# Performance work log

Measured on AMD Instinct MI355X. Metric: run time of the kernel, lower is better.

Reference implementation:

```python
import jax, jax.numpy as jnp
import numpy as np

INV_SQRT2 = 0.7071067811865476  # Haar/db1 filter coefficient
LEVEL = 3


def _split(x, axis):
    """One Haar analysis step along `axis` (even length assumed)."""
    ax = axis % x.ndim
    sl0 = [slice(None)] * x.ndim; sl0[ax] = slice(0, None, 2)
    sl1 = [slice(None)] * x.ndim; sl1[ax] = slice(1, None, 2)
    x0, x1 = x[tuple(sl0)], x[tuple(sl1)]
    return (x0 + x1) * INV_SQRT2, (x0 - x1) * INV_SQRT2


def _merge(lo, hi, axis):
    """One Haar synthesis step along `axis` (interleave even/odd)."""
    ax = axis % lo.ndim
    e = (lo + hi) * INV_SQRT2
    o = (lo - hi) * INV_SQRT2
    s = jnp.stack([e, o], axis=ax + 1)
    shape = list(lo.shape)
    shape[ax] *= 2
    return s.reshape(shape)


def _dwt2(x):
    lo, hi = _split(x, -1)
    a, h = _split(lo, -2)
    v, d = _split(hi, -2)
    return a, h, v, d


def _idwt2(a, h, v, d):
    lo = _merge(a, h, -2)
    hi = _merge(v, d, -2)
    return _merge(lo, hi, -1)


def setup_inputs() -> dict:
    key = jax.random.key(0)
    ks = jax.random.split(key, 8)
    B, H, W = 16, 1024, 1024
    x = jax.random.normal(ks[0], (B, H, W, 1), dtype=jnp.float32)
    na = (H // 8) * (W // 8)   # approx size at level 3
    n2 = (H // 4) * (W // 4)
    n1 = (H // 2) * (W // 2)
    scale = 0.02
    Wa = jax.random.normal(ks[1], (na, 1), dtype=jnp.float32) * scale
    ba = jnp.zeros((1,), jnp.float32)
    Wd1 = jax.random.normal(ks[2], (3 * na, 3), dtype=jnp.float32) * scale  # coarsest details
    bd1 = jnp.zeros((3,), jnp.float32)
    Wd2 = jax.random.normal(ks[3], (3 * n2, 3), dtype=jnp.float32) * scale
    bd2 = jnp.zeros((3,), jnp.float32)
    Wd3 = jax.random.normal(ks[4], (3 * n1, 3), dtype=jnp.float32) * scale  # finest details
    bd3 = jnp.zeros((3,), jnp.float32)
    return {"x": x, "Wa": Wa, "ba": ba, "Wd1": Wd1, "bd1": bd1,
            "Wd2": Wd2, "bd2": bd2, "Wd3": Wd3, "bd3": bd3}


def reference(x, Wa, ba, Wd1, bd1, Wd2, bd2, Wd3, bd3):
    img = x[..., 0]                      # [B, H, W]
    B = img.shape[0]
    details = []                         # finest -> coarsest
    cur = img
    for _ in range(LEVEL):
        cur, h, v, d = _dwt2(cur)
        details.append((h, v, d))
    # approximation attention: sigmoid(Dense(1)) scalar gate per sample
    aw = jax.nn.sigmoid(cur.reshape(B, -1) @ Wa + ba)   # [B, 1]
    rec = cur * aw[:, :, None]                           # [B, H/8, W/8]
    # detail attention per level (coarsest first, matching pywt coeff order)
    det_params = [(Wd1, bd1), (Wd2, bd2), (Wd3, bd3)]
    for (h, v, d), (Wd, bd) in zip(reversed(details), det_params):
        flat = jnp.stack([h, v, d], axis=1).reshape(B, -1)      # [B, 3*hl*wl]
        w = jax.nn.softmax(flat @ Wd + bd, axis=-1)             # [B, 3]
        rec = _idwt2(rec,
                     h * w[:, 0, None, None],
                     v * w[:, 1, None, None],
                     d * w[:, 2, None, None])
    return rec                                                   # [B, H, W]
```

## Files before the change

kernel.cpp:

```cpp
#include <hip/hip_runtime.h>
#include <math.h>

#define HH 1024
#define WW 1024
#define N1 262144
#define N2 65536
#define N3 16384
#define NCHUNK 4
#define ROWS_PER_IMG 512

#define C_INV_SQRT2 0.70710678118654752440f

static __device__ __forceinline__ void haar_fwd(float P, float Q, float R, float S,
                                                float& a, float& h, float& v, float& d) {
    const float C = C_INV_SQRT2;
    float lo0 = (P + Q) * C, lo1 = (R + S) * C;
    float hi0 = (P - Q) * C, hi1 = (R - S) * C;
    a = (lo0 + lo1) * C; h = (lo0 - lo1) * C;
    v = (hi0 + hi1) * C; d = (hi0 - hi1) * C;
}

static __device__ __forceinline__ void haar_inv(float a, float h, float v, float d,
                                                float& P, float& Q, float& R, float& S) {
    const float C = C_INV_SQRT2;
    float elo = (a + h) * C, olo = (a - h) * C;
    float ehi = (v + d) * C, ohi = (v - d) * C;
    P = (elo + ehi) * C; Q = (elo - ehi) * C;
    R = (olo + ohi) * C; S = (olo - ohi) * C;
}

__global__ __launch_bounds__(256) void wa_fwd_dots(
    const float* __restrict__ x,
    const float* __restrict__ Wa,
    const float* __restrict__ Wd1,
    const float* __restrict__ Wd2,
    const float* __restrict__ Wd3,
    float* __restrict__ partial,
    int ipc)
{
    const int strip = blockIdx.x;
    const int chunk = blockIdx.y;
    const int t = threadIdx.x;
    const int lane = t & 63, wave = t >> 6;

    float w1[3][4][6];
    #pragma unroll
    for (int qr = 0; qr < 4; ++qr) {
        const size_t jj = (size_t)(strip * 4 + qr) * 512 + 2 * t;
        #pragma unroll
        for (int s = 0; s < 3; ++s) {
            const float2* src = (const float2*)(Wd3 + (jj + (size_t)s * N1) * 3);
            float2 f0 = src[0], f1 = src[1], f2 = src[2];
            w1[s][qr][0] = f0.x; w1[s][qr][1] = f0.y; w1[s][qr][2] = f1.x;
            w1[s][qr][3] = f1.y; w1[s][qr][4] = f2.x; w1[s][qr][5] = f2.y;
        }
    }
    float w2[3][2][3];
    #pragma unroll
    for (int QR = 0; QR < 2; ++QR) {
        const size_t jj = (size_t)(strip * 2 + QR) * 256 + t;
        #pragma unroll
        for (int s = 0; s < 3; ++s) {
            const float* src = Wd2 + (jj + (size_t)s * N2) * 3;
            w2[s][QR][0] = src[0]; w2[s][QR][1] = src[1]; w2[s][QR][2] = src[2];
        }
    }
    float w3[3][3] = {};
    float wa = 0.f;
    if (!(t & 1)) {
        const size_t jj = (size_t)strip * 128 + (t >> 1);
        wa = Wa[jj];
        #pragma unroll
        for (int s = 0; s < 3; ++s) {
            const float* src = Wd1 + (jj + (size_t)s * N3) * 3;
            w3[s][0] = src[0]; w3[s][1] = src[1]; w3[s][2] = src[2];
        }
    }

    #pragma unroll 2
    for (int bi = 0; bi < ipc; ++bi) {
        const int b = chunk * ipc + bi;
        const float* xr = x + (size_t)b * HH * WW + (size_t)strip * 8 * WW + 4 * t;

        float acc[10];
        #pragma unroll
        for (int c = 0; c < 10; ++c) acc[c] = 0.f;

        float a1[4][2];
        #pragma unroll
        for (int qr = 0; qr < 4; ++qr) {
            float4 u0 = *(const float4*)(xr + (size_t)(2 * qr)     * WW);
            float4 u1 = *(const float4*)(xr + (size_t)(2 * qr + 1) * WW);
            float h_[2], v_[2], d_[2];
            haar_fwd(u0.x, u0.y, u1.x, u1.y, a1[qr][0], h_[0], v_[0], d_[0]);
            haar_fwd(u0.z, u0.w, u1.z, u1.w, a1[qr][1], h_[1], v_[1], d_[1]);
            #pragma unroll
            for (int qc = 0; qc < 2; ++qc)
                #pragma unroll
                for (int c = 0; c < 3; ++c)
                    acc[7 + c] += h_[qc] * w1[0][qr][qc * 3 + c]
                                + v_[qc] * w1[1][qr][qc * 3 + c]
                                + d_[qc] * w1[2][qr][qc * 3 + c];
        }

        float a2[2];
        #pragma unroll
        for (int QR = 0; QR < 2; ++QR) {
            float h2, v2, d2;
            haar_fwd(a1[2 * QR][0], a1[2 * QR][1], a1[2 * QR + 1][0], a1[2 * QR + 1][1],
                     a2[QR], h2, v2, d2);
            #pragma unroll
            for (int c = 0; c < 3; ++c)
                acc[4 + c] += h2 * w2[0][QR][c] + v2 * w2[1][QR][c] + d2 * w2[2][QR][c];
        }

        {
            float oa0 = __shfl_xor(a2[0], 1);
            float oa1 = __shfl_xor(a2[1], 1);
            if (!(t & 1)) {
                float a3, h3, v3, d3;
                haar_fwd(a2[0], oa0, a2[1], oa1, a3, h3, v3, d3);
                acc[0] += a3 * wa;
                #pragma unroll
                for (int c = 0; c < 3; ++c)
                    acc[1 + c] += h3 * w3[0][c] + v3 * w3[1][c] + d3 * w3[2][c];
            }
        }

        #pragma unroll
        for (int c = 0; c < 10; ++c) {
            float s = acc[c];
            #pragma unroll
            for (int off = 1; off < 64; off <<= 1) s += __shfl_xor(s, off);
            acc[c] = s;
        }
        if (lane == 0) {
            float* row = partial + ((size_t)b * ROWS_PER_IMG + (size_t)strip * 4 + wave) * 10;
            #pragma unroll
            for (int c = 0; c < 10; ++c) row[c] = acc[c];
        }
    }
}

__global__ __launch_bounds__(64) void wa_gates(
    const float* __restrict__ partial,
    const float* __restrict__ ba,
    const float* __restrict__ bd1,
    const float* __restrict__ bd2,
    const float* __restrict__ bd3,
    float* __restrict__ gates)
{
    const int b = blockIdx.x;
    const int l = threadIdx.x;
    float v[10];
    #pragma unroll
    for (int c = 0; c < 10; ++c) v[c] = 0.f;
    for (int r = l; r < ROWS_PER_IMG; r += 64) {
        const float* row = partial + ((size_t)b * ROWS_PER_IMG + r) * 10;
        #pragma unroll
        for (int c = 0; c < 10; ++c) v[c] += row[c];
    }
    #pragma unroll
    for (int c = 0; c < 10; ++c) {
        #pragma unroll
        for (int off = 1; off < 64; off <<= 1) v[c] += __shfl_xor(v[c], off);
    }
    if (l == 0) {
        float* G = gates + b * 10;
        G[0] = 1.f / (1.f + expf(-(v[0] + ba[0])));
        const float* bds[3] = { bd1, bd2, bd3 };
        #pragma unroll
        for (int lv = 0; lv < 3; ++lv) {
            float l0 = v[1 + 3 * lv + 0] + bds[lv][0];
            float l1 = v[1 + 3 * lv + 1] + bds[lv][1];
            float l2 = v[1 + 3 * lv + 2] + bds[lv][2];
            float m = fmaxf(l0, fmaxf(l1, l2));
            float e0 = expf(l0 - m), e1 = expf(l1 - m), e2 = expf(l2 - m);
            float inv = 1.f / (e0 + e1 + e2);
            G[1 + 3 * lv + 0] = e0 * inv;
            G[1 + 3 * lv + 1] = e1 * inv;
            G[1 + 3 * lv + 2] = e2 * inv;
        }
    }
}

__global__ __launch_bounds__(256) void wa_recon(
    const float* __restrict__ x,
    const float* __restrict__ gates,
    float* __restrict__ out)
{
    const int strip = blockIdx.x;
    const int b = blockIdx.y;
    const int t = threadIdx.x;

    __shared__ float g[10];
    if (t < 10) g[t] = gates[b * 10 + t];
    __syncthreads();

    const float* xr = x + (size_t)b * HH * WW + (size_t)strip * 8 * WW + 4 * t;

    float a1[4][2], h1[4][2], v1[4][2], d1[4][2];
    #pragma unroll
    for (int qr = 0; qr < 4; ++qr) {
        float4 u0 = *(const float4*)(xr + (size_t)(2 * qr)     * WW);
        float4 u1 = *(const float4*)(xr + (size_t)(2 * qr + 1) * WW);
        haar_fwd(u0.x, u0.y, u1.x, u1.y, a1[qr][0], h1[qr][0], v1[qr][0], d1[qr][0]);
        haar_fwd(u0.z, u0.w, u1.z, u1.w, a1[qr][1], h1[qr][1], v1[qr][1], d1[qr][1]);
    }
    float a2[2], h2[2], v2[2], d2[2];
    #pragma unroll
    for (int QR = 0; QR < 2; ++QR)
        haar_fwd(a1[2 * QR][0], a1[2 * QR][1], a1[2 * QR + 1][0], a1[2 * QR + 1][1],
                 a2[QR], h2[QR], v2[QR], d2[QR]);

    float oa0 = __shfl_xor(a2[0], 1);
    float oa1 = __shfl_xor(a2[1], 1);
    const bool rightside = t & 1;
    float a3, h3, v3, d3;
    if (!rightside) haar_fwd(a2[0], oa0, a2[1], oa1, a3, h3, v3, d3);
    else            haar_fwd(oa0, a2[0], oa1, a2[1], a3, h3, v3, d3);

    a3 *= g[0];
    float P, Q, R, S;
    haar_inv(a3, h3 * g[1], v3 * g[2], d3 * g[3], P, Q, R, S);
    float r2[2];
    r2[0] = rightside ? Q : P;
    r2[1] = rightside ? S : R;

    float ra1[4][2];
    #pragma unroll
    for (int QR = 0; QR < 2; ++QR) {
        haar_inv(r2[QR], h2[QR] * g[4], v2[QR] * g[5], d2[QR] * g[6], P, Q, R, S);
        ra1[2 * QR][0] = P; ra1[2 * QR][1] = Q;
        ra1[2 * QR + 1][0] = R; ra1[2 * QR + 1][1] = S;
    }

    float* orow = out + (size_t)b * HH * WW + (size_t)strip * 8 * WW + 4 * t;
    #pragma unroll
    for (int qr = 0; qr < 4; ++qr) {
        float4 o0, o1;
        haar_inv(ra1[qr][0], h1[qr][0] * g[7], v1[qr][0] * g[8], d1[qr][0] * g[9],
                 o0.x, o0.y, o1.x, o1.y);
        haar_inv(ra1[qr][1], h1[qr][1] * g[7], v1[qr][1] * g[8], d1[qr][1] * g[9],
                 o0.z, o0.w, o1.z, o1.w);
        *(float4*)(orow + (size_t)(2 * qr)     * WW) = o0;
        *(float4*)(orow + (size_t)(2 * qr + 1) * WW) = o1;
    }
}

extern "C" void kernel_launch(void* const* d_in, const int* in_sizes, int n_in,
                              void* d_out, int out_size, void* d_ws, size_t ws_size,
                              hipStream_t stream) {
    const float* x   = (const float*)d_in[0];
    const float* Wa  = (const float*)d_in[1];
    const float* ba  = (const float*)d_in[2];
    const float* Wd1 = (const float*)d_in[3];
    const float* bd1 = (const float*)d_in[4];
    const float* Wd2 = (const float*)d_in[5];
    const float* bd2 = (const float*)d_in[6];
    const float* Wd3 = (const float*)d_in[7];
    const float* bd3 = (const float*)d_in[8];
    float* out = (float*)d_out;

    const int B = in_sizes[0] / (HH * WW);

    float* partial = (float*)d_ws;
    float* gates   = partial + (size_t)B * ROWS_PER_IMG * 10;

    int nchunk = NCHUNK, ipc = B / NCHUNK;
    if (B % NCHUNK) { nchunk = B; ipc = 1; }

    dim3 fgrid(128, nchunk);
    wa_fwd_dots<<<fgrid, 256, 0, stream>>>(x, Wa, Wd1, Wd2, Wd3, partial, ipc);
    wa_gates<<<B, 64, 0, stream>>>(partial, ba, bd1, bd2, bd3, gates);
    dim3 rgrid(128, B);
    wa_recon<<<rgrid, 256, 0, stream>>>(x, gates, out);
}
```

Before: 155.7 us.

## Fuse forward dots, gates and reconstruction into one cooperative kernel

```diff
diff --git a/kernel.cpp b/kernel.cpp
--- a/kernel.cpp
+++ b/kernel.cpp
@@ -1,5 +1,8 @@
 #include <hip/hip_runtime.h>
+#include <hip/hip_cooperative_groups.h>
 #include <math.h>
+
+namespace cg = cooperative_groups;
 
 #define HH 1024
 #define WW 1024
@@ -7,7 +10,7 @@
 #define N2 65536
 #define N3 16384
 #define NCHUNK 4
-#define ROWS_PER_IMG 512
+#define ROWS_PER_IMG 128
 
 #define C_INV_SQRT2 0.70710678118654752440f
 
@@ -27,6 +30,227 @@
     float ehi = (v + d) * C, ohi = (v - d) * C;
     P = (elo + ehi) * C; Q = (elo - ehi) * C;
     R = (olo + ohi) * C; S = (olo - ohi) * C;
+}
+
+static __device__ __forceinline__ void gates_from_partials(
+    const float* __restrict__ partial, int b, int lane,
+    const float* __restrict__ ba, const float* __restrict__ bd1,
+    const float* __restrict__ bd2, const float* __restrict__ bd3,
+    float* gdst)
+{
+    const float* base = partial + (size_t)b * ROWS_PER_IMG * 10 + lane * 20;
+    float v[10];
+    #pragma unroll
+    for (int c = 0; c < 10; ++c) v[c] = base[c] + base[10 + c];
+    #pragma unroll
+    for (int c = 0; c < 10; ++c) {
+        #pragma unroll
+        for (int off = 1; off < 64; off <<= 1) v[c] += __shfl_xor(v[c], off);
+    }
+    if (lane == 0) {
+        gdst[0] = 1.f / (1.f + expf(-(v[0] + ba[0])));
+        const float* bds[3] = { bd1, bd2, bd3 };
+        #pragma unroll
+        for (int lv = 0; lv < 3; ++lv) {
+            float l0 = v[1 + 3 * lv + 0] + bds[lv][0];
+            float l1 = v[1 + 3 * lv + 1] + bds[lv][1];
+            float l2 = v[1 + 3 * lv + 2] + bds[lv][2];
+            float m = fmaxf(l0, fmaxf(l1, l2));
+            float e0 = expf(l0 - m), e1 = expf(l1 - m), e2 = expf(l2 - m);
+            float inv = 1.f / (e0 + e1 + e2);
+            gdst[1 + 3 * lv + 0] = e0 * inv;
+            gdst[1 + 3 * lv + 1] = e1 * inv;
+            gdst[1 + 3 * lv + 2] = e2 * inv;
+        }
+    }
+}
+
+__global__ __launch_bounds__(256) void wa_fused(
+    const float* __restrict__ x,
+    const float* __restrict__ Wa,
+    const float* __restrict__ ba,
+    const float* __restrict__ bd1,
+    const float* __restrict__ bd2,
+    const float* __restrict__ bd3,
+    const float* __restrict__ Wd1,
+    const float* __restrict__ Wd2,
+    const float* __restrict__ Wd3,
+    float* __restrict__ out,
+    float* __restrict__ partial,
+    int ipc)
+{
+    const int strip = blockIdx.x;
+    const int chunk = blockIdx.y;
+    const int t = threadIdx.x;
+    const int lane = t & 63, wave = t >> 6;
+
+    __shared__ float red[4][10];
+    __shared__ float g_lds[16][10];
+
+    float w1[3][4][6];
+    #pragma unroll
+    for (int qr = 0; qr < 4; ++qr) {
+        const size_t jj = (size_t)(strip * 4 + qr) * 512 + 2 * t;
+        #pragma unroll
+        for (int s = 0; s < 3; ++s) {
+            const float2* src = (const float2*)(Wd3 + (jj + (size_t)s * N1) * 3);
+            float2 f0 = src[0], f1 = src[1], f2 = src[2];
+            w1[s][qr][0] = f0.x; w1[s][qr][1] = f0.y; w1[s][qr][2] = f1.x;
+            w1[s][qr][3] = f1.y; w1[s][qr][4] = f2.x; w1[s][qr][5] = f2.y;
+        }
+    }
+    float w2[3][2][3];
+    #pragma unroll
+    for (int QR = 0; QR < 2; ++QR) {
+        const size_t jj = (size_t)(strip * 2 + QR) * 256 + t;
+        #pragma unroll
+        for (int s = 0; s < 3; ++s) {
+            const float* src = Wd2 + (jj + (size_t)s * N2) * 3;
+            w2[s][QR][0] = src[0]; w2[s][QR][1] = src[1]; w2[s][QR][2] = src[2];
+        }
+    }
+    float w3[3][3] = {};
+    float wa = 0.f;
+    if (!(t & 1)) {
+        const size_t jj = (size_t)strip * 128 + (t >> 1);
+        wa = Wa[jj];
+        #pragma unroll
+        for (int s = 0; s < 3; ++s) {
+            const float* src = Wd1 + (jj + (size_t)s * N3) * 3;
+            w3[s][0] = src[0]; w3[s][1] = src[1]; w3[s][2] = src[2];
+        }
+    }
+
+    for (int bi = 0; bi < ipc; ++bi) {
+        const int b = chunk * ipc + bi;
+        const float* xr = x + (size_t)b * HH * WW + (size_t)strip * 8 * WW + 4 * t;
+
+        float acc[10];
+        #pragma unroll
+        for (int c = 0; c < 10; ++c) acc[c] = 0.f;
+
+        float a1[4][2];
+        #pragma unroll
+        for (int qr = 0; qr < 4; ++qr) {
+            float4 u0 = *(const float4*)(xr + (size_t)(2 * qr)     * WW);
+            float4 u1 = *(const float4*)(xr + (size_t)(2 * qr + 1) * WW);
+            float h_[2], v_[2], d_[2];
+            haar_fwd(u0.x, u0.y, u1.x, u1.y, a1[qr][0], h_[0], v_[0], d_[0]);
+            haar_fwd(u0.z, u0.w, u1.z, u1.w, a1[qr][1], h_[1], v_[1], d_[1]);
+            #pragma unroll
+            for (int qc = 0; qc < 2; ++qc)
+                #pragma unroll
+                for (int c = 0; c < 3; ++c)
+                    acc[7 + c] += h_[qc] * w1[0][qr][qc * 3 + c]
+                                + v_[qc] * w1[1][qr][qc * 3 + c]
+                                + d_[qc] * w1[2][qr][qc * 3 + c];
+        }
+
+        float a2[2];
+        #pragma unroll
+        for (int QR = 0; QR < 2; ++QR) {
+            float h2, v2, d2;
+            haar_fwd(a1[2 * QR][0], a1[2 * QR][1], a1[2 * QR + 1][0], a1[2 * QR + 1][1],
+                     a2[QR], h2, v2, d2);
+            #pragma unroll
+            for (int c = 0; c < 3; ++c)
+                acc[4 + c] += h2 * w2[0][QR][c] + v2 * w2[1][QR][c] + d2 * w2[2][QR][c];
+        }
+
+        {
+            float oa0 = __shfl_xor(a2[0], 1);
+            float oa1 = __shfl_xor(a2[1], 1);
+            if (!(t & 1)) {
+                float a3, h3, v3, d3;
+                haar_fwd(a2[0], oa0, a2[1], oa1, a3, h3, v3, d3);
+                acc[0] += a3 * wa;
+                #pragma unroll
+                for (int c = 0; c < 3; ++c)
+                    acc[1 + c] += h3 * w3[0][c] + v3 * w3[1][c] + d3 * w3[2][c];
+            }
+        }
+
+        #pragma unroll
+        for (int c = 0; c < 10; ++c) {
+            float s = acc[c];
+            #pragma unroll
+            for (int off = 1; off < 64; off <<= 1) s += __shfl_xor(s, off);
+            acc[c] = s;
+        }
+        if (lane == 0) {
+            #pragma unroll
+            for (int c = 0; c < 10; ++c) red[wave][c] = acc[c];
+        }
+        __syncthreads();
+        if (t < 10)
+            partial[((size_t)b * ROWS_PER_IMG + strip) * 10 + t] =
+                red[0][t] + red[1][t] + red[2][t] + red[3][t];
+        __syncthreads();
+    }
+
+    __threadfence();
+    cg::this_grid().sync();
+
+    for (int bi = wave; bi < ipc; bi += 4)
+        gates_from_partials(partial, chunk * ipc + bi, lane, ba, bd1, bd2, bd3, g_lds[bi]);
+    __syncthreads();
+
+    for (int bi = 0; bi < ipc; ++bi) {
+        const int b = chunk * ipc + bi;
+        float g[10];
+        #pragma unroll
+        for (int c = 0; c < 10; ++c) g[c] = g_lds[bi][c];
+
+        const float* xr = x + (size_t)b * HH * WW + (size_t)strip * 8 * WW + 4 * t;
+
+        float a1[4][2], h1[4][2], v1[4][2], d1[4][2];
+        #pragma unroll
+        for (int qr = 0; qr < 4; ++qr) {
+            float4 u0 = *(const float4*)(xr + (size_t)(2 * qr)     * WW);
+            float4 u1 = *(const float4*)(xr + (size_t)(2 * qr + 1) * WW);
+            haar_fwd(u0.x, u0.y, u1.x, u1.y, a1[qr][0], h1[qr][0], v1[qr][0], d1[qr][0]);
+            haar_fwd(u0.z, u0.w, u1.z, u1.w, a1[qr][1], h1[qr][1], v1[qr][1], d1[qr][1]);
+        }
+        float a2[2], h2[2], v2[2], d2[2];
+        #pragma unroll
+        for (int QR = 0; QR < 2; ++QR)
+            haar_fwd(a1[2 * QR][0], a1[2 * QR][1], a1[2 * QR + 1][0], a1[2 * QR + 1][1],
+                     a2[QR], h2[QR], v2[QR], d2[QR]);
+
+        float oa0 = __shfl_xor(a2[0], 1);
+        float oa1 = __shfl_xor(a2[1], 1);
+        const bool rightside = t & 1;
+        float a3, h3, v3, d3;
+        if (!rightside) haar_fwd(a2[0], oa0, a2[1], oa1, a3, h3, v3, d3);
+        else            haar_fwd(oa0, a2[0], oa1, a2[1], a3, h3, v3, d3);
+
+        a3 *= g[0];
+        float P, Q, R, S;
+        haar_inv(a3, h3 * g[1], v3 * g[2], d3 * g[3], P, Q, R, S);
+        float r2[2];
+        r2[0] = rightside ? Q : P;
+        r2[1] = rightside ? S : R;
+
+        float ra1[4][2];
+        #pragma unroll
+        for (int QR = 0; QR < 2; ++QR) {
+            haar_inv(r2[QR], h2[QR] * g[4], v2[QR] * g[5], d2[QR] * g[6], P, Q, R, S);
+            ra1[2 * QR][0] = P; ra1[2 * QR][1] = Q;
+            ra1[2 * QR + 1][0] = R; ra1[2 * QR + 1][1] = S;
+        }
+
+        float* orow = out + (size_t)b * HH * WW + (size_t)strip * 8 * WW + 4 * t;
+        #pragma unroll
+        for (int qr = 0; qr < 4; ++qr) {
+            float4 o0, o1;
+            haar_inv(ra1[qr][0], h1[qr][0] * g[7], v1[qr][0] * g[8], d1[qr][0] * g[9],
+                     o0.x, o0.y, o1.x, o1.y);
+            haar_inv(ra1[qr][1], h1[qr][1] * g[7], v1[qr][1] * g[8], d1[qr][1] * g[9],
+                     o0.z, o0.w, o1.z, o1.w);
+            *(float4*)(orow + (size_t)(2 * qr)     * WW) = o0;
+            *(float4*)(orow + (size_t)(2 * qr + 1) * WW) = o1;
+        }
+    }
 }
 
 __global__ __launch_bounds__(256) void wa_fwd_dots(
@@ -43,6 +267,8 @@
     const int t = threadIdx.x;
     const int lane = t & 63, wave = t >> 6;
 
+    __shared__ float red[4][10];
+
     float w1[3][4][6];
     #pragma unroll
     for (int qr = 0; qr < 4; ++qr) {
@@ -77,7 +303,6 @@
         }
     }
 
-    #pragma unroll 2
     for (int bi = 0; bi < ipc; ++bi) {
         const int b = chunk * ipc + bi;
         const float* xr = x + (size_t)b * HH * WW + (size_t)strip * 8 * WW + 4 * t;
@@ -135,10 +360,14 @@
             acc[c] = s;
         }
         if (lane == 0) {
-            float* row = partial + ((size_t)b * ROWS_PER_IMG + (size_t)strip * 4 + wave) * 10;
-            #pragma unroll
-            for (int c = 0; c < 10; ++c) row[c] = acc[c];
-        }
+            #pragma unroll
+            for (int c = 0; c < 10; ++c) red[wave][c] = acc[c];
+        }
+        __syncthreads();
+        if (t < 10)
+            partial[((size_t)b * ROWS_PER_IMG + strip) * 10 + t] =
+                red[0][t] + red[1][t] + red[2][t] + red[3][t];
+        __syncthreads();
     }
 }
 
@@ -150,38 +379,8 @@
     const float* __restrict__ bd3,
     float* __restrict__ gates)
 {
-    const int b = blockIdx.x;
-    const int l = threadIdx.x;
-    float v[10];
-    #pragma unroll
-    for (int c = 0; c < 10; ++c) v[c] = 0.f;
-    for (int r = l; r < ROWS_PER_IMG; r += 64) {
-        const float* row = partial + ((size_t)b * ROWS_PER_IMG + r) * 10;
-        #pragma unroll
-        for (int c = 0; c < 10; ++c) v[c] += row[c];
-    }
-    #pragma unroll
-    for (int c = 0; c < 10; ++c) {
-        #pragma unroll
-        for (int off = 1; off < 64; off <<= 1) v[c] += __shfl_xor(v[c], off);
-    }
-    if (l == 0) {
-        float* G = gates + b * 10;
-        G[0] = 1.f / (1.f + expf(-(v[0] + ba[0])));
-        const float* bds[3] = { bd1, bd2, bd3 };
-        #pragma unroll
-        for (int lv = 0; lv < 3; ++lv) {
-            float l0 = v[1 + 3 * lv + 0] + bds[lv][0];
-            float l1 = v[1 + 3 * lv + 1] + bds[lv][1];
-            float l2 = v[1 + 3 * lv + 2] + bds[lv][2];
-            float m = fmaxf(l0, fmaxf(l1, l2));
-            float e0 = expf(l0 - m), e1 = expf(l1 - m), e2 = expf(l2 - m);
-            float inv = 1.f / (e0 + e1 + e2);
-            G[1 + 3 * lv + 0] = e0 * inv;
-            G[1 + 3 * lv + 1] = e1 * inv;
-            G[1 + 3 * lv + 2] = e2 * inv;
-        }
-    }
+    gates_from_partials(partial, blockIdx.x, threadIdx.x, ba, bd1, bd2, bd3,
+                        gates + blockIdx.x * 10);
 }
 
 __global__ __launch_bounds__(256) void wa_recon(
@@ -268,11 +467,20 @@
     float* gates   = partial + (size_t)B * ROWS_PER_IMG * 10;
 
     int nchunk = NCHUNK, ipc = B / NCHUNK;
-    if (B % NCHUNK) { nchunk = B; ipc = 1; }
-
-    dim3 fgrid(128, nchunk);
-    wa_fwd_dots<<<fgrid, 256, 0, stream>>>(x, Wa, Wd1, Wd2, Wd3, partial, ipc);
-    wa_gates<<<B, 64, 0, stream>>>(partial, ba, bd1, bd2, bd3, gates);
-    dim3 rgrid(128, B);
-    wa_recon<<<rgrid, 256, 0, stream>>>(x, gates, out);
-}
+    if (B % NCHUNK || B > 64) { nchunk = B; ipc = 1; }
+
+    void* args[] = { (void*)&x, (void*)&Wa, (void*)&ba, (void*)&bd1, (void*)&bd2,
+                     (void*)&bd3, (void*)&Wd1, (void*)&Wd2, (void*)&Wd3,
+                     (void*)&out, (void*)&partial, (void*)&ipc };
+    hipError_t err = hipLaunchCooperativeKernel(
+        reinterpret_cast<void*>(wa_fused), dim3(128, nchunk), dim3(256),
+        args, 0, stream);
+
+    if (err != hipSuccess) {
+        dim3 fgrid(128, nchunk);
+        wa_fwd_dots<<<fgrid, 256, 0, stream>>>(x, Wa, Wd1, Wd2, Wd3, partial, ipc);
+        wa_gates<<<B, 64, 0, stream>>>(partial, ba, bd1, bd2, bd3, gates);
+        dim3 rgrid(128, B);
+        wa_recon<<<rgrid, 256, 0, stream>>>(x, gates, out);
+    }
+}
```

Measured after the change: 263.7 us. 69.4% more time.
